# Performance work log

Hardware: AMD Instinct MI355X
Metric: run time of the kernel (lower is better)

Reference implementation:

```python
import jax, jax.numpy as jnp
import numpy as np

N_NODES = 50000


def gcn_conv(x, W, b, src, dst):
    # PyG GCNConv: lin (no bias) -> add self-loops -> symmetric deg norm ->
    # scatter-add messages to target nodes -> add bias.
    n = x.shape[0]
    xw = x @ W  # [N, H]
    loops = jnp.arange(n, dtype=src.dtype)
    s = jnp.concatenate([src, loops])
    d = jnp.concatenate([dst, loops])
    deg = jax.ops.segment_sum(jnp.ones(d.shape[0], dtype=x.dtype), d, num_segments=n)
    dinv = deg ** -0.5  # deg >= 1 due to self-loops
    norm = dinv[s] * dinv[d]  # [E+N]
    msg = xw[s] * norm[:, None]  # gather + scale, [E+N, H]
    out = jax.ops.segment_sum(msg, d, num_segments=n)  # scatter-add
    return out + b


def setup_inputs() -> dict:
    key = jax.random.key(0)
    ks = jax.random.split(key, 8)
    in_feats, hidden, out_feats, p = 64, 64, 32, 4
    x = jax.random.normal(ks[0], (N_NODES, in_feats), dtype=jnp.float32)
    edge_index = jax.random.randint(ks[1], (2, 800000), 0, N_NODES, dtype=jnp.int64)
    s1 = (1.0 / in_feats) ** 0.5
    s2 = (1.0 / hidden) ** 0.5
    W1 = jax.random.uniform(ks[2], (in_feats, hidden), jnp.float32, -s1, s1)
    b1 = jnp.zeros((hidden,), jnp.float32)
    W2 = jax.random.uniform(ks[3], (hidden, hidden), jnp.float32, -s2, s2)
    b2 = jnp.zeros((hidden,), jnp.float32)
    Wr = jax.random.uniform(ks[4], (hidden, out_feats * p), jnp.float32, -s2, s2)
    br = jax.random.uniform(ks[5], (out_feats * p,), jnp.float32, -s2, s2)
    return {"x": x, "edge_index": edge_index, "W1": W1, "b1": b1,
            "W2": W2, "b2": b2, "Wr": Wr, "br": br}


def reference(x, edge_index, W1, b1, W2, b2, Wr, br):
    src, dst = edge_index[0], edge_index[1]
    h = jax.nn.relu(gcn_conv(x, W1, b1, src, dst))
    h = jax.nn.relu(gcn_conv(h, W2, b2, src, dst))
    g = jnp.mean(h, axis=0, keepdims=True)  # [1, hidden]
    out = (g @ Wr + br).reshape(32, 4)  # (out_feats, p)
    return out
```

## Files before the change

kernel.cpp:

```cpp
#include <hip/hip_runtime.h>
#include <math.h>


#define CH 4096
#define MAXNB 1024

__global__ __launch_bounds__(256) void k_bucket_hist(const int* __restrict__ dst,
                                                     int* __restrict__ histmat,
                                                     int E, int NB) {
    __shared__ int ih[MAXNB];
    int t = threadIdx.x;
    for (int k = t; k < NB; k += 256) ih[k] = 0;
    __syncthreads();
    int base = blockIdx.x * CH;
    for (int i = 0; i < CH; i += 256) {
        int e = base + i + t;
        if (e < E) atomicAdd(&ih[dst[e] >> 6], 1);
    }
    __syncthreads();
    for (int k = t; k < NB; k += 256) histmat[(size_t)blockIdx.x * NB + k] = ih[k];
}

__global__ __launch_bounds__(256) void k_colscan(int* __restrict__ histmat,
                                                 int* __restrict__ tot,
                                                 int NB, int nch) {
    int k = blockIdx.x * 256 + threadIdx.x;
    if (k >= NB) return;
    int run = 0;
    int b = 0;
    for (; b + 8 <= nch; b += 8) {
        int v[8];
#pragma unroll
        for (int u = 0; u < 8; u++) v[u] = histmat[(size_t)(b + u) * NB + k];
#pragma unroll
        for (int u = 0; u < 8; u++) {
            int x = v[u];
            histmat[(size_t)(b + u) * NB + k] = run;
            run += x;
        }
    }
    for (; b < nch; b++) {
        int x = histmat[(size_t)b * NB + k];
        histmat[(size_t)b * NB + k] = run;
        run += x;
    }
    tot[k] = run;
}

__global__ __launch_bounds__(256) void k_scanb(const int* __restrict__ tot,
                                               int* __restrict__ bstart,
                                               int* __restrict__ offsets,
                                               int NB, int E, int n) {
    __shared__ int sc[256];
    __shared__ int carry;
    int t = threadIdx.x;
    if (t == 0) carry = 0;
    __syncthreads();
    int nchunk = (NB + 255) / 256;
    for (int c = 0; c < nchunk; c++) {
        int idx = c * 256 + t;
        int v = (idx < NB) ? tot[idx] : 0;
        sc[t] = v;
        __syncthreads();
        for (int off = 1; off < 256; off <<= 1) {
            int x = (t >= off) ? sc[t - off] : 0;
            __syncthreads();
            sc[t] += x;
            __syncthreads();
        }
        if (idx < NB) bstart[idx] = sc[t] - v + carry;
        __syncthreads();
        if (t == 0) carry += sc[255];
        __syncthreads();
    }
    if (t == 0) { bstart[NB] = E; offsets[n] = E; }
}

__global__ __launch_bounds__(256) void k_bucket_scatter(const int* __restrict__ src,
                                                        const int* __restrict__ dst,
                                                        const int* __restrict__ histmat,
                                                        const int* __restrict__ bstart,
                                                        int* __restrict__ staged,
                                                        int E, int NB) {
    __shared__ int cur[MAXNB];
    int t = threadIdx.x;
    for (int k = t; k < NB; k += 256)
        cur[k] = bstart[k] + histmat[(size_t)blockIdx.x * NB + k];
    __syncthreads();
    int base = blockIdx.x * CH;
    for (int i = 0; i < CH; i += 256) {
        int e = base + i + t;
        if (e < E) {
            int d = dst[e];
            int pos = atomicAdd(&cur[d >> 6], 1);
            staged[pos] = (src[e] << 6) | (d & 63);
        }
    }
}

__global__ __launch_bounds__(256) void k_local_sort(const int* __restrict__ staged,
                                                    const int* __restrict__ bstart,
                                                    unsigned short* __restrict__ csr,
                                                    int* __restrict__ offsets,
                                                    float* __restrict__ dinv, int n) {
    __shared__ int cnt[64];
    __shared__ int pos[64];
    __shared__ int cur[64];
    int t = threadIdx.x;
    if (t < 64) cnt[t] = 0;
    __syncthreads();
    int k = blockIdx.x;
    int beg = bstart[k], end = bstart[k + 1];
    for (int e = beg + t; e < end; e += 256) atomicAdd(&cnt[staged[e] & 63], 1);
    __syncthreads();
    if (t == 0) {
        int run = 0;
        for (int i = 0; i < 64; i++) { pos[i] = run; run += cnt[i]; }
    }
    __syncthreads();
    if (t < 64) {
        cur[t] = pos[t];
        int node = k * 64 + t;
        if (node < n) {
            offsets[node] = beg + pos[t];
            dinv[node] = 1.0f / sqrtf((float)(cnt[t] + 1));
        }
    }
    __syncthreads();
    for (int e = beg + t; e < end; e += 256) {
        int pk = staged[e];
        int p = atomicAdd(&cur[pk & 63], 1);
        csr[beg + p] = (unsigned short)(pk >> 6);
    }
}

template <bool QIN>
__global__ __launch_bounds__(256) void k_gemm_scale(const float* __restrict__ X,
                                                    const float* __restrict__ W,
                                                    const float* __restrict__ dinv,
                                                    float* __restrict__ Y, int n) {
    __shared__ float Ws[64 * 64];
    __shared__ float xs[16][64];
    int t = threadIdx.x, w = t >> 6, f = t & 63;
    const float4* W4 = (const float4*)W;
    float4* Ws4 = (float4*)Ws;
#pragma unroll
    for (int j = 0; j < 4; j++) Ws4[t + 256 * j] = W4[t + 256 * j];
    int r0 = blockIdx.x * 16;
#pragma unroll
    for (int i = 0; i < 4; i++) {
        int r = r0 + w * 4 + i;
        float v = 0.f;
        if (r < n)
            v = QIN ? X[((size_t)(f >> 4) * n + r) * 16 + (f & 15)]
                    : X[(size_t)r * 64 + f];
        xs[w * 4 + i][f] = v;
    }
    __syncthreads();
    float acc[4] = {0.f, 0.f, 0.f, 0.f};
#pragma unroll 8
    for (int k = 0; k < 64; k++) {
        float wv = Ws[k * 64 + f];
#pragma unroll
        for (int i = 0; i < 4; i++) acc[i] += xs[w * 4 + i][k] * wv;
    }
#pragma unroll
    for (int i = 0; i < 4; i++) {
        int r = r0 + w * 4 + i;
        if (r < n) Y[((size_t)(f >> 4) * n + r) * 16 + (f & 15)] = dinv[r] * acc[i];
    }
}

__device__ __forceinline__ float4 xor4(float4 a, int m) {
    a.x += __shfl_xor(a.x, m);
    a.y += __shfl_xor(a.y, m);
    a.z += __shfl_xor(a.z, m);
    a.w += __shfl_xor(a.w, m);
    return a;
}

template <bool POOL>
__global__ __launch_bounds__(256) void k_aggregate_q(const float* __restrict__ Y,
                                                     const float* __restrict__ dinv,
                                                     const float* __restrict__ bias,
                                                     const int* __restrict__ offsets,
                                                     const unsigned short* __restrict__ csr,
                                                     float* __restrict__ Yout,
                                                     float* __restrict__ pbuf,
                                                     int n, int nblk) {
    __shared__ float4 sm4[4][4];
    int t = threadIdx.x, w = t >> 6, l = t & 63;
    int i = l >> 4, j = (l >> 2) & 3, c = l & 3;
    int pass = blockIdx.x / nblk, blk = blockIdx.x - pass * nblk;
    int node = blk * 16 + w * 4 + i;
    const float4* Y4 = (const float4*)Y + (size_t)pass * n * 4;
    bool valid = node < n;
    float4 acc = make_float4(0.f, 0.f, 0.f, 0.f);
    float dv = 0.f;
    if (valid) {
        int beg = offsets[node];
        int deg = offsets[node + 1] - beg;
        dv = dinv[node];
        if (j == 0) acc = Y4[(size_t)node * 4 + c];
        for (int e0 = 0; e0 < deg; e0 += 16) {
#pragma unroll
            for (int u = 0; u < 4; u++) {
                int e = e0 + u * 4 + j;
                if (e < deg) {
                    int s = csr[beg + e];
                    float4 v = Y4[(size_t)s * 4 + c];
                    acc.x += v.x; acc.y += v.y; acc.z += v.z; acc.w += v.w;
                }
            }
        }
    }
    acc = xor4(acc, 4);
    acc = xor4(acc, 8);
    float4 b4 = ((const float4*)bias)[pass * 4 + c];
    float4 h = make_float4(0.f, 0.f, 0.f, 0.f);
    if (valid) {
        h.x = fmaxf(dv * acc.x + b4.x, 0.f);
        h.y = fmaxf(dv * acc.y + b4.y, 0.f);
        h.z = fmaxf(dv * acc.z + b4.z, 0.f);
        h.w = fmaxf(dv * acc.w + b4.w, 0.f);
    }
    if (!POOL) {
        if (valid && j == 0)
            ((float4*)Yout + (size_t)pass * n * 4)[(size_t)node * 4 + c] = h;
    } else {
        h = xor4(h, 16);
        h = xor4(h, 32);
        if (l < 4) sm4[w][c] = h;
        __syncthreads();
        if (t < 4) {
            float4 a = sm4[0][t], b = sm4[1][t], d = sm4[2][t], e = sm4[3][t];
            float4 s;
            s.x = (a.x + b.x) + (d.x + e.x);
            s.y = (a.y + b.y) + (d.y + e.y);
            s.z = (a.z + b.z) + (d.z + e.z);
            s.w = (a.w + b.w) + (d.w + e.w);
            ((float4*)pbuf)[((size_t)blk * 4 + pass) * 4 + t] = s;
        }
    }
}

__global__ void k_mean_final(const float* __restrict__ pbuf, float* __restrict__ g,
                             int nrows) {
    __shared__ float part[256];
    int t = threadIdx.x, w = t >> 6, f = t & 63;
    float local = 0.f;
    for (int r = blockIdx.x * 4 + w; r < nrows; r += gridDim.x * 4)
        local += pbuf[(size_t)r * 64 + f];
    part[t] = local;
    __syncthreads();
    if (w == 0) {
        float tot = part[f] + part[64 + f] + part[128 + f] + part[192 + f];
        atomicAdd(&g[f], tot);
    }
}

__global__ void k_readout(const float* __restrict__ g, const float* __restrict__ Wr,
                          const float* __restrict__ br, float* __restrict__ out,
                          float invn) {
    __shared__ float gl[64];
    int t = threadIdx.x;
    if (t < 64) gl[t] = g[t] * invn;
    __syncthreads();
    float acc = br[t];
#pragma unroll
    for (int k = 0; k < 64; k++) acc += gl[k] * Wr[k * 128 + t];
    out[t] = acc;
}

extern "C" void kernel_launch(void* const* d_in, const int* in_sizes, int n_in,
                              void* d_out, int out_size, void* d_ws, size_t ws_size,
                              hipStream_t stream) {
    const float* x  = (const float*)d_in[0];
    const int*   ei = (const int*)d_in[1];
    const float* W1 = (const float*)d_in[2];
    const float* b1 = (const float*)d_in[3];
    const float* W2 = (const float*)d_in[4];
    const float* b2 = (const float*)d_in[5];
    const float* Wr = (const float*)d_in[6];
    const float* br = (const float*)d_in[7];
    float* out = (float*)d_out;

    int n = in_sizes[0] / 64;
    int E = in_sizes[1] / 2;
    const int* src = ei;
    const int* dst = ei + E;

    int NB   = (n + 63) / 64;
    int nch  = (E + CH - 1) / CH;
    int nblk = (n + 15) / 16;

    char* p = (char*)d_ws;
    float* y1 = (float*)p;     p += (size_t)n * 64 * sizeof(float);
    float* y2 = (float*)p;     p += (size_t)n * 64 * sizeof(float);
    float* dinv = (float*)p;   p += (size_t)n * sizeof(float);
    float* g = (float*)p;      p += 64 * sizeof(float);
    int* staged = (int*)p;     p += (size_t)E * sizeof(int);
    int* offsets = (int*)p;    p += (size_t)(n + 1) * sizeof(int);
    int* histmat = (int*)p;    p += (size_t)nch * NB * sizeof(int);
    int* tot = (int*)p;        p += (size_t)NB * sizeof(int);
    int* bstart = (int*)p;     p += (size_t)(NB + 1) * sizeof(int);
    unsigned short* csr = (unsigned short*)p; p += (size_t)E * sizeof(unsigned short);

    hipMemsetAsync(g, 0, 64 * sizeof(float), stream);
    k_bucket_hist<<<nch, 256, 0, stream>>>(dst, histmat, E, NB);
    k_colscan<<<(NB + 255) / 256, 256, 0, stream>>>(histmat, tot, NB, nch);
    k_scanb<<<1, 256, 0, stream>>>(tot, bstart, offsets, NB, E, n);
    k_bucket_scatter<<<nch, 256, 0, stream>>>(src, dst, histmat, bstart, staged, E, NB);
    k_local_sort<<<NB, 256, 0, stream>>>(staged, bstart, csr, offsets, dinv, n);

    k_gemm_scale<false><<<(n + 15) / 16, 256, 0, stream>>>(x, W1, dinv, y1, n);
    k_aggregate_q<false><<<4 * nblk, 256, 0, stream>>>(y1, dinv, b1, offsets, csr,
                                                       y2, nullptr, n, nblk);
    k_gemm_scale<true><<<(n + 15) / 16, 256, 0, stream>>>(y2, W2, dinv, y1, n);
    float* pbuf = y2;
    k_aggregate_q<true><<<4 * nblk, 256, 0, stream>>>(y1, dinv, b2, offsets, csr,
                                                      nullptr, pbuf, n, nblk);

    k_mean_final<<<64, 256, 0, stream>>>(pbuf, g, nblk);
    k_readout<<<1, 128, 0, stream>>>(g, Wr, br, out, 1.0f / (float)n);
}
```

Baseline: 233.7 us.

## Fuse CSR build into cooperative kernel and fuse aggregation with layer-2 GEMM

Merges the five CSR-construction kernels into one cooperative kernel with grid-wide syncs over 256 blocks. Layer-1 aggregation is fused with the layer-2 GEMM, and the final aggregation pools straight into g with atomics, which removes the separate mean kernel and the memset. The aggregation layout moves from a 4-pass quarter-feature scheme to row-major float4 with 16 lanes per node. The goals are fewer launches and less intermediate traffic, but the build now runs on only 256 blocks and the gathers for each node are serial per lane.

```diff
diff --git a/kernel.cpp b/kernel.cpp
--- a/kernel.cpp
+++ b/kernel.cpp
@@ -1,140 +1,122 @@
 #include <hip/hip_runtime.h>
+#include <hip/hip_cooperative_groups.h>
 #include <math.h>
 
-
-#define CH 4096
+namespace cg = cooperative_groups;
+
+
 #define MAXNB 1024
-
-__global__ __launch_bounds__(256) void k_bucket_hist(const int* __restrict__ dst,
-                                                     int* __restrict__ histmat,
-                                                     int E, int NB) {
-    __shared__ int ih[MAXNB];
-    int t = threadIdx.x;
-    for (int k = t; k < NB; k += 256) ih[k] = 0;
-    __syncthreads();
-    int base = blockIdx.x * CH;
-    for (int i = 0; i < CH; i += 256) {
-        int e = base + i + t;
-        if (e < E) atomicAdd(&ih[dst[e] >> 6], 1);
-    }
-    __syncthreads();
-    for (int k = t; k < NB; k += 256) histmat[(size_t)blockIdx.x * NB + k] = ih[k];
-}
-
-__global__ __launch_bounds__(256) void k_colscan(int* __restrict__ histmat,
-                                                 int* __restrict__ tot,
-                                                 int NB, int nch) {
-    int k = blockIdx.x * 256 + threadIdx.x;
-    if (k >= NB) return;
-    int run = 0;
-    int b = 0;
-    for (; b + 8 <= nch; b += 8) {
-        int v[8];
-#pragma unroll
-        for (int u = 0; u < 8; u++) v[u] = histmat[(size_t)(b + u) * NB + k];
-#pragma unroll
-        for (int u = 0; u < 8; u++) {
-            int x = v[u];
-            histmat[(size_t)(b + u) * NB + k] = run;
-            run += x;
-        }
-    }
-    for (; b < nch; b++) {
-        int x = histmat[(size_t)b * NB + k];
-        histmat[(size_t)b * NB + k] = run;
-        run += x;
-    }
-    tot[k] = run;
-}
-
-__global__ __launch_bounds__(256) void k_scanb(const int* __restrict__ tot,
+#define GB 256
+
+__global__ __launch_bounds__(256) void k_build(const int* __restrict__ src,
+                                               const int* __restrict__ dst,
+                                               int* __restrict__ histmat,
+                                               int* __restrict__ tot,
                                                int* __restrict__ bstart,
+                                               int* __restrict__ staged,
+                                               unsigned short* __restrict__ csr,
                                                int* __restrict__ offsets,
-                                               int NB, int E, int n) {
+                                               float* __restrict__ dinv,
+                                               float* __restrict__ g,
+                                               int E, int n, int NB, int CH2) {
+    cg::grid_group grid = cg::this_grid();
+    __shared__ int sm[MAXNB];
     __shared__ int sc[256];
     __shared__ int carry;
-    int t = threadIdx.x;
-    if (t == 0) carry = 0;
-    __syncthreads();
-    int nchunk = (NB + 255) / 256;
-    for (int c = 0; c < nchunk; c++) {
-        int idx = c * 256 + t;
-        int v = (idx < NB) ? tot[idx] : 0;
-        sc[t] = v;
-        __syncthreads();
-        for (int off = 1; off < 256; off <<= 1) {
-            int x = (t >= off) ? sc[t - off] : 0;
+    __shared__ int cnt[64], pref[64], cur[64];
+    int t = threadIdx.x, b = blockIdx.x;
+    if (b == 0 && t < 64) g[t] = 0.f;
+
+    for (int k = t; k < NB; k += 256) sm[k] = 0;
+    __syncthreads();
+    int base = b * CH2;
+    int lim = min(E, base + CH2);
+    for (int e = base + t; e < lim; e += 256) atomicAdd(&sm[dst[e] >> 6], 1);
+    __syncthreads();
+    for (int k = t; k < NB; k += 256) histmat[(size_t)b * NB + k] = sm[k];
+    grid.sync();
+
+    int kk = b * 256 + t;
+    if (kk < NB) {
+        int run = 0;
+        for (int c = 0; c < GB; c += 8) {
+            int v[8];
+#pragma unroll
+            for (int u = 0; u < 8; u++) v[u] = histmat[(size_t)(c + u) * NB + kk];
+#pragma unroll
+            for (int u = 0; u < 8; u++) {
+                int x = v[u];
+                histmat[(size_t)(c + u) * NB + kk] = run;
+                run += x;
+            }
+        }
+        tot[kk] = run;
+    }
+    grid.sync();
+
+    if (b == 0) {
+        if (t == 0) carry = 0;
+        __syncthreads();
+        int nchunk = (NB + 255) / 256;
+        for (int c = 0; c < nchunk; c++) {
+            int idx = c * 256 + t;
+            int v = (idx < NB) ? tot[idx] : 0;
+            sc[t] = v;
             __syncthreads();
-            sc[t] += x;
+            for (int off = 1; off < 256; off <<= 1) {
+                int x = (t >= off) ? sc[t - off] : 0;
+                __syncthreads();
+                sc[t] += x;
+                __syncthreads();
+            }
+            if (idx < NB) bstart[idx] = sc[t] - v + carry;
             __syncthreads();
-        }
-        if (idx < NB) bstart[idx] = sc[t] - v + carry;
-        __syncthreads();
-        if (t == 0) carry += sc[255];
-        __syncthreads();
-    }
-    if (t == 0) { bstart[NB] = E; offsets[n] = E; }
-}
-
-__global__ __launch_bounds__(256) void k_bucket_scatter(const int* __restrict__ src,
-                                                        const int* __restrict__ dst,
-                                                        const int* __restrict__ histmat,
-                                                        const int* __restrict__ bstart,
-                                                        int* __restrict__ staged,
-                                                        int E, int NB) {
-    __shared__ int cur[MAXNB];
-    int t = threadIdx.x;
+            if (t == 0) carry += sc[255];
+            __syncthreads();
+        }
+        if (t == 0) { bstart[NB] = E; offsets[n] = E; }
+    }
+    grid.sync();
+
     for (int k = t; k < NB; k += 256)
-        cur[k] = bstart[k] + histmat[(size_t)blockIdx.x * NB + k];
-    __syncthreads();
-    int base = blockIdx.x * CH;
-    for (int i = 0; i < CH; i += 256) {
-        int e = base + i + t;
-        if (e < E) {
-            int d = dst[e];
-            int pos = atomicAdd(&cur[d >> 6], 1);
-            staged[pos] = (src[e] << 6) | (d & 63);
-        }
-    }
-}
-
-__global__ __launch_bounds__(256) void k_local_sort(const int* __restrict__ staged,
-                                                    const int* __restrict__ bstart,
-                                                    unsigned short* __restrict__ csr,
-                                                    int* __restrict__ offsets,
-                                                    float* __restrict__ dinv, int n) {
-    __shared__ int cnt[64];
-    __shared__ int pos[64];
-    __shared__ int cur[64];
-    int t = threadIdx.x;
-    if (t < 64) cnt[t] = 0;
-    __syncthreads();
-    int k = blockIdx.x;
-    int beg = bstart[k], end = bstart[k + 1];
-    for (int e = beg + t; e < end; e += 256) atomicAdd(&cnt[staged[e] & 63], 1);
-    __syncthreads();
-    if (t == 0) {
-        int run = 0;
-        for (int i = 0; i < 64; i++) { pos[i] = run; run += cnt[i]; }
-    }
-    __syncthreads();
-    if (t < 64) {
-        cur[t] = pos[t];
-        int node = k * 64 + t;
-        if (node < n) {
-            offsets[node] = beg + pos[t];
-            dinv[node] = 1.0f / sqrtf((float)(cnt[t] + 1));
-        }
-    }
-    __syncthreads();
-    for (int e = beg + t; e < end; e += 256) {
-        int pk = staged[e];
-        int p = atomicAdd(&cur[pk & 63], 1);
-        csr[beg + p] = (unsigned short)(pk >> 6);
-    }
-}
-
-template <bool QIN>
+        sm[k] = bstart[k] + histmat[(size_t)b * NB + k];
+    __syncthreads();
+    for (int e = base + t; e < lim; e += 256) {
+        int d = dst[e];
+        int pos = atomicAdd(&sm[d >> 6], 1);
+        staged[pos] = (src[e] << 6) | (d & 63);
+    }
+    grid.sync();
+
+    for (int k = b; k < NB; k += gridDim.x) {
+        if (t < 64) cnt[t] = 0;
+        __syncthreads();
+        int beg = bstart[k], end = bstart[k + 1];
+        for (int e = beg + t; e < end; e += 256) atomicAdd(&cnt[staged[e] & 63], 1);
+        __syncthreads();
+        if (t == 0) {
+            int run = 0;
+            for (int i = 0; i < 64; i++) { pref[i] = run; run += cnt[i]; }
+        }
+        __syncthreads();
+        if (t < 64) {
+            cur[t] = pref[t];
+            int node = k * 64 + t;
+            if (node < n) {
+                offsets[node] = beg + pref[t];
+                dinv[node] = 1.0f / sqrtf((float)(cnt[t] + 1));
+            }
+        }
+        __syncthreads();
+        for (int e = beg + t; e < end; e += 256) {
+            int pk = staged[e];
+            int p = atomicAdd(&cur[pk & 63], 1);
+            csr[beg + p] = (unsigned short)(pk >> 6);
+        }
+        __syncthreads();
+    }
+}
+
 __global__ __launch_bounds__(256) void k_gemm_scale(const float* __restrict__ X,
                                                     const float* __restrict__ W,
                                                     const float* __restrict__ dinv,
@@ -150,11 +132,7 @@
 #pragma unroll
     for (int i = 0; i < 4; i++) {
         int r = r0 + w * 4 + i;
-        float v = 0.f;
-        if (r < n)
-            v = QIN ? X[((size_t)(f >> 4) * n + r) * 16 + (f & 15)]
-                    : X[(size_t)r * 64 + f];
-        xs[w * 4 + i][f] = v;
+        xs[w * 4 + i][f] = (r < n) ? X[(size_t)r * 64 + f] : 0.f;
     }
     __syncthreads();
     float acc[4] = {0.f, 0.f, 0.f, 0.f};
@@ -167,7 +145,7 @@
 #pragma unroll
     for (int i = 0; i < 4; i++) {
         int r = r0 + w * 4 + i;
-        if (r < n) Y[((size_t)(f >> 4) * n + r) * 16 + (f & 15)] = dinv[r] * acc[i];
+        if (r < n) Y[(size_t)r * 64 + f] = dinv[r] * acc[i];
     }
 }
 
@@ -179,83 +157,114 @@
     return a;
 }
 
-template <bool POOL>
-__global__ __launch_bounds__(256) void k_aggregate_q(const float* __restrict__ Y,
-                                                     const float* __restrict__ dinv,
-                                                     const float* __restrict__ bias,
-                                                     const int* __restrict__ offsets,
-                                                     const unsigned short* __restrict__ csr,
-                                                     float* __restrict__ Yout,
-                                                     float* __restrict__ pbuf,
-                                                     int n, int nblk) {
-    __shared__ float4 sm4[4][4];
+__global__ __launch_bounds__(256) void k_agg_fuse(const float* __restrict__ Y,
+                                                  const float* __restrict__ dinv,
+                                                  const float* __restrict__ bias,
+                                                  const int* __restrict__ offsets,
+                                                  const unsigned short* __restrict__ csr,
+                                                  const float* __restrict__ W2,
+                                                  float* __restrict__ Yout, int n) {
+    __shared__ float Ws[64 * 64];
+    __shared__ float hs[16 * 64];
     int t = threadIdx.x, w = t >> 6, l = t & 63;
-    int i = l >> 4, j = (l >> 2) & 3, c = l & 3;
-    int pass = blockIdx.x / nblk, blk = blockIdx.x - pass * nblk;
-    int node = blk * 16 + w * 4 + i;
-    const float4* Y4 = (const float4*)Y + (size_t)pass * n * 4;
+    int i = l >> 4, c = l & 15;
+    const float4* W4 = (const float4*)W2;
+    float4* Ws4 = (float4*)Ws;
+#pragma unroll
+    for (int j = 0; j < 4; j++) Ws4[t + 256 * j] = W4[t + 256 * j];
+    int base = blockIdx.x * 16;
+    int node = base + w * 4 + i;
     bool valid = node < n;
+    const float4* Y4 = (const float4*)Y;
     float4 acc = make_float4(0.f, 0.f, 0.f, 0.f);
-    float dv = 0.f;
     if (valid) {
+        acc = Y4[(size_t)node * 16 + c];
         int beg = offsets[node];
         int deg = offsets[node + 1] - beg;
-        dv = dinv[node];
-        if (j == 0) acc = Y4[(size_t)node * 4 + c];
-        for (int e0 = 0; e0 < deg; e0 += 16) {
-#pragma unroll
-            for (int u = 0; u < 4; u++) {
-                int e = e0 + u * 4 + j;
+        for (int e0 = 0; e0 < deg; e0 += 8) {
+#pragma unroll
+            for (int u = 0; u < 8; u++) {
+                int e = e0 + u;
                 if (e < deg) {
                     int s = csr[beg + e];
-                    float4 v = Y4[(size_t)s * 4 + c];
+                    float4 v = Y4[(size_t)s * 16 + c];
                     acc.x += v.x; acc.y += v.y; acc.z += v.z; acc.w += v.w;
                 }
             }
         }
-    }
-    acc = xor4(acc, 4);
-    acc = xor4(acc, 8);
-    float4 b4 = ((const float4*)bias)[pass * 4 + c];
-    float4 h = make_float4(0.f, 0.f, 0.f, 0.f);
+        float dv = dinv[node];
+        float4 b4 = ((const float4*)bias)[c];
+        acc.x = fmaxf(dv * acc.x + b4.x, 0.f);
+        acc.y = fmaxf(dv * acc.y + b4.y, 0.f);
+        acc.z = fmaxf(dv * acc.z + b4.z, 0.f);
+        acc.w = fmaxf(dv * acc.w + b4.w, 0.f);
+    } else {
+        acc = make_float4(0.f, 0.f, 0.f, 0.f);
+    }
+    ((float4*)hs)[(w * 4 + i) * 16 + c] = acc;
+    __syncthreads();
+    float a2[4] = {0.f, 0.f, 0.f, 0.f};
+    int f = l;
+#pragma unroll 8
+    for (int k = 0; k < 64; k++) {
+        float wv = Ws[k * 64 + f];
+#pragma unroll
+        for (int r = 0; r < 4; r++) a2[r] += hs[(w * 4 + r) * 64 + k] * wv;
+    }
+#pragma unroll
+    for (int r = 0; r < 4; r++) {
+        int rr = base + w * 4 + r;
+        if (rr < n) Yout[(size_t)rr * 64 + f] = dinv[rr] * a2[r];
+    }
+}
+
+__global__ __launch_bounds__(256) void k_agg_pool(const float* __restrict__ Y,
+                                                  const float* __restrict__ dinv,
+                                                  const float* __restrict__ bias,
+                                                  const int* __restrict__ offsets,
+                                                  const unsigned short* __restrict__ csr,
+                                                  float* __restrict__ g, int n) {
+    __shared__ float4 sm4[4][16];
+    int t = threadIdx.x, w = t >> 6, l = t & 63;
+    int i = l >> 4, c = l & 15;
+    int node = blockIdx.x * 16 + w * 4 + i;
+    bool valid = node < n;
+    const float4* Y4 = (const float4*)Y;
+    float4 acc = make_float4(0.f, 0.f, 0.f, 0.f);
     if (valid) {
-        h.x = fmaxf(dv * acc.x + b4.x, 0.f);
-        h.y = fmaxf(dv * acc.y + b4.y, 0.f);
-        h.z = fmaxf(dv * acc.z + b4.z, 0.f);
-        h.w = fmaxf(dv * acc.w + b4.w, 0.f);
-    }
-    if (!POOL) {
-        if (valid && j == 0)
-            ((float4*)Yout + (size_t)pass * n * 4)[(size_t)node * 4 + c] = h;
+        acc = Y4[(size_t)node * 16 + c];
+        int beg = offsets[node];
+        int deg = offsets[node + 1] - beg;
+        for (int e0 = 0; e0 < deg; e0 += 8) {
+#pragma unroll
+            for (int u = 0; u < 8; u++) {
+                int e = e0 + u;
+                if (e < deg) {
+                    int s = csr[beg + e];
+                    float4 v = Y4[(size_t)s * 16 + c];
+                    acc.x += v.x; acc.y += v.y; acc.z += v.z; acc.w += v.w;
+                }
+            }
+        }
+        float dv = dinv[node];
+        float4 b4 = ((const float4*)bias)[c];
+        acc.x = fmaxf(dv * acc.x + b4.x, 0.f);
+        acc.y = fmaxf(dv * acc.y + b4.y, 0.f);
+        acc.z = fmaxf(dv * acc.z + b4.z, 0.f);
+        acc.w = fmaxf(dv * acc.w + b4.w, 0.f);
     } else {
-        h = xor4(h, 16);
-        h = xor4(h, 32);
-        if (l < 4) sm4[w][c] = h;
-        __syncthreads();
-        if (t < 4) {
-            float4 a = sm4[0][t], b = sm4[1][t], d = sm4[2][t], e = sm4[3][t];
-            float4 s;
-            s.x = (a.x + b.x) + (d.x + e.x);
-            s.y = (a.y + b.y) + (d.y + e.y);
-            s.z = (a.z + b.z) + (d.z + e.z);
-            s.w = (a.w + b.w) + (d.w + e.w);
-            ((float4*)pbuf)[((size_t)blk * 4 + pass) * 4 + t] = s;
-        }
-    }
-}
-
-__global__ void k_mean_final(const float* __restrict__ pbuf, float* __restrict__ g,
-                             int nrows) {
-    __shared__ float part[256];
-    int t = threadIdx.x, w = t >> 6, f = t & 63;
-    float local = 0.f;
-    for (int r = blockIdx.x * 4 + w; r < nrows; r += gridDim.x * 4)
-        local += pbuf[(size_t)r * 64 + f];
-    part[t] = local;
-    __syncthreads();
-    if (w == 0) {
-        float tot = part[f] + part[64 + f] + part[128 + f] + part[192 + f];
-        atomicAdd(&g[f], tot);
+        acc = make_float4(0.f, 0.f, 0.f, 0.f);
+    }
+    acc = xor4(acc, 16);
+    acc = xor4(acc, 32);
+    if (l < 16) sm4[w][l] = acc;
+    __syncthreads();
+    if (t < 16) {
+        float4 a = sm4[0][t], b = sm4[1][t], d = sm4[2][t], e = sm4[3][t];
+        atomicAdd(&g[t * 4 + 0], (a.x + b.x) + (d.x + e.x));
+        atomicAdd(&g[t * 4 + 1], (a.y + b.y) + (d.y + e.y));
+        atomicAdd(&g[t * 4 + 2], (a.z + b.z) + (d.z + e.z));
+        atomicAdd(&g[t * 4 + 3], (a.w + b.w) + (d.w + e.w));
     }
 }
 
@@ -290,9 +299,8 @@
     const int* src = ei;
     const int* dst = ei + E;
 
-    int NB   = (n + 63) / 64;
-    int nch  = (E + CH - 1) / CH;
-    int nblk = (n + 15) / 16;
+    int NB  = (n + 63) / 64;
+    int CH2 = (E + GB - 1) / GB;
 
     char* p = (char*)d_ws;
     float* y1 = (float*)p;     p += (size_t)n * 64 * sizeof(float);
@@ -301,26 +309,18 @@
     float* g = (float*)p;      p += 64 * sizeof(float);
     int* staged = (int*)p;     p += (size_t)E * sizeof(int);
     int* offsets = (int*)p;    p += (size_t)(n + 1) * sizeof(int);
-    int* histmat = (int*)p;    p += (size_t)nch * NB * sizeof(int);
+    int* histmat = (int*)p;    p += (size_t)GB * NB * sizeof(int);
     int* tot = (int*)p;        p += (size_t)NB * sizeof(int);
     int* bstart = (int*)p;     p += (size_t)(NB + 1) * sizeof(int);
     unsigned short* csr = (unsigned short*)p; p += (size_t)E * sizeof(unsigned short);
 
-    hipMemsetAsync(g, 0, 64 * sizeof(float), stream);
-    k_bucket_hist<<<nch, 256, 0, stream>>>(dst, histmat, E, NB);
-    k_colscan<<<(NB + 255) / 256, 256, 0, stream>>>(histmat, tot, NB, nch);
-    k_scanb<<<1, 256, 0, stream>>>(tot, bstart, offsets, NB, E, n);
-    k_bucket_scatter<<<nch, 256, 0, stream>>>(src, dst, histmat, bstart, staged, E, NB);
-    k_local_sort<<<NB, 256, 0, stream>>>(staged, bstart, csr, offsets, dinv, n);
-
-    k_gemm_scale<false><<<(n + 15) / 16, 256, 0, stream>>>(x, W1, dinv, y1, n);
-    k_aggregate_q<false><<<4 * nblk, 256, 0, stream>>>(y1, dinv, b1, offsets, csr,
-                                                       y2, nullptr, n, nblk);
-    k_gemm_scale<true><<<(n + 15) / 16, 256, 0, stream>>>(y2, W2, dinv, y1, n);
-    float* pbuf = y2;
-    k_aggregate_q<true><<<4 * nblk, 256, 0, stream>>>(y1, dinv, b2, offsets, csr,
-                                                      nullptr, pbuf, n, nblk);
-
-    k_mean_final<<<64, 256, 0, stream>>>(pbuf, g, nblk);
+    void* bargs[] = {&src, &dst, &histmat, &tot, &bstart, &staged, &csr,
+                     &offsets, &dinv, &g, &E, &n, &NB, &CH2};
+    hipLaunchCooperativeKernel((void*)k_build, dim3(GB), dim3(256), bargs, 0, stream);
+
+    int nblk = (n + 15) / 16;
+    k_gemm_scale<<<nblk, 256, 0, stream>>>(x, W1, dinv, y1, n);
+    k_agg_fuse<<<nblk, 256, 0, stream>>>(y1, dinv, b1, offsets, csr, W2, y2, n);
+    k_agg_pool<<<nblk, 256, 0, stream>>>(y2, dinv, b2, offsets, csr, g, n);
     k_readout<<<1, 128, 0, stream>>>(g, Wr, br, out, 1.0f / (float)n);
 }
```

Result: slower. 558.9 us (+139.2%).
